# Performance work log

Measured on AMD Instinct MI355X. Metric: run time of the kernel, lower is better.

Reference implementation:

```python
import jax, jax.numpy as jnp
import numpy as np
import math

N = 100000      # nodes
DEG = 16        # fixed avg degree
E = N * DEG     # edges (nnz)
DIN = 128
DOUT = 32


def setup_inputs() -> dict:
    key = jax.random.key(0)
    k1, k2, k3, k4 = jax.random.split(key, 4)
    H = jax.random.normal(k1, (N, DIN), dtype=jnp.float32)
    stdv = 1.0 / math.sqrt(DOUT)
    weight = jax.random.uniform(k2, (DIN, DOUT), dtype=jnp.float32, minval=-stdv, maxval=stdv)
    # CSR adjacency: fixed degree per row -> rowPtr is an arithmetic sequence
    rowPtr = (jnp.arange(N + 1, dtype=jnp.int32) * DEG)
    colIdx = jax.random.randint(k3, (E,), 0, N, dtype=jnp.int32)
    val = jax.random.uniform(k4, (E,), dtype=jnp.float32)  # normalized edge weights
    return {"H": H, "weight": weight, "rowPtr": rowPtr, "colIdx": colIdx, "val": val}


def reference(H, weight, rowPtr, colIdx, val):
    # GCN layer: H' = A @ (H @ W), A sparse in CSR.
    HW = H @ weight                                   # [N, DOUT] dense GEMM
    n_rows = rowPtr.shape[0] - 1
    deg = jnp.diff(rowPtr)
    # expand CSR rowPtr to per-edge row ids (static total length -> jit-safe)
    rows = jnp.repeat(jnp.arange(n_rows, dtype=jnp.int32), deg,
                      total_repeat_length=colIdx.shape[0])
    msgs = HW[colIdx] * val[:, None]                  # [E, DOUT] gather + scale
    return jax.ops.segment_sum(msgs, rows, num_segments=n_rows)  # SpMM scatter-add
```

## Files before the change

kernel.cpp:

```cpp
#include <hip/hip_runtime.h>

#define DIN  128
#define DOUT 32

typedef __attribute__((ext_vector_type(8))) short bf16x8;
typedef __attribute__((ext_vector_type(4))) float f32x4;

__device__ __forceinline__ unsigned int f2b(float f) {
    unsigned int u = __float_as_uint(f);
    return (u + 0x7fffu + ((u >> 16) & 1u)) >> 16;
}
__device__ __forceinline__ unsigned int cvtpk(float lo, float hi) {
    unsigned int r;
    asm("v_cvt_pk_bf16_f32 %0, %1, %2" : "=v"(r) : "v"(lo), "v"(hi));
    return r;
}

union FragU { bf16x8 v; unsigned int u[4]; };

__global__ __launch_bounds__(256) void gemm_mfma_kernel(
    const float* __restrict__ H, const float* __restrict__ W,
    unsigned short* __restrict__ HWb, int n)
{
    const int lane = threadIdx.x & 63;
    const int w    = threadIdx.x >> 6;
    int rb = blockIdx.x * 128 + w * 32;
    if (rb + 32 > n) rb = n - 32;
    const int lr = lane & 15;
    const int kh = lane >> 4;

    bf16x8 bfrag[2][4];
    #pragma unroll
    for (int ct = 0; ct < 2; ++ct) {
        #pragma unroll
        for (int ks = 0; ks < 4; ++ks) {
            const int col = ct * 16 + lr;
            const int k0  = ks * 32 + kh * 8;
            float f[8];
            #pragma unroll
            for (int j = 0; j < 8; ++j) f[j] = W[(k0 + j) * DOUT + col];
            FragU fu;
            fu.u[0] = cvtpk(f[0], f[1]); fu.u[1] = cvtpk(f[2], f[3]);
            fu.u[2] = cvtpk(f[4], f[5]); fu.u[3] = cvtpk(f[6], f[7]);
            bfrag[ct][ks] = fu.v;
        }
    }

    f32x4 acc[2][2];
    #pragma unroll
    for (int rt = 0; rt < 2; ++rt)
        #pragma unroll
        for (int ct = 0; ct < 2; ++ct)
            acc[rt][ct] = (f32x4){0.f, 0.f, 0.f, 0.f};

    #pragma unroll
    for (int rt = 0; rt < 2; ++rt) {
        const float* __restrict__ hp = H + (size_t)(rb + rt * 16 + lr) * DIN;
        bf16x8 afrag[4];
        #pragma unroll
        for (int ks = 0; ks < 4; ++ks) {
            const int k0 = ks * 32 + kh * 8;
            const float4 lo = *reinterpret_cast<const float4*>(hp + k0);
            const float4 hi = *reinterpret_cast<const float4*>(hp + k0 + 4);
            FragU fu;
            fu.u[0] = cvtpk(lo.x, lo.y); fu.u[1] = cvtpk(lo.z, lo.w);
            fu.u[2] = cvtpk(hi.x, hi.y); fu.u[3] = cvtpk(hi.z, hi.w);
            afrag[ks] = fu.v;
        }
        #pragma unroll
        for (int ct = 0; ct < 2; ++ct)
            #pragma unroll
            for (int ks = 0; ks < 4; ++ks)
                acc[rt][ct] = __builtin_amdgcn_mfma_f32_16x16x32_bf16(
                    afrag[ks], bfrag[ct][ks], acc[rt][ct], 0, 0, 0);
    }

    #pragma unroll
    for (int rt = 0; rt < 2; ++rt) {
        #pragma unroll
        for (int ct = 0; ct < 2; ++ct) {
            #pragma unroll
            for (int r = 0; r < 4; ++r) {
                const int row = rb + rt * 16 + kh * 4 + r;
                const int col = ct * 16 + lr;
                HWb[(size_t)row * DOUT + col] = (unsigned short)f2b(acc[rt][ct][r]);
            }
        }
    }
}

__global__ __launch_bounds__(256) void spmm_kernel(
    const unsigned short* __restrict__ HWb, const int* __restrict__ rowPtr,
    const int* __restrict__ colIdx, const float* __restrict__ val,
    float* __restrict__ out, int n)
{
    const uint4* __restrict__ tbl = reinterpret_cast<const uint4*>(HWb);
    const int gid = blockIdx.x * 256 + threadIdx.x;
    const int row = gid >> 2;
    if (row >= n) return;
    const int cg = gid & 3;

    const int start = rowPtr[row];
    const int end   = rowPtr[row + 1];
    float a0=0,a1=0,a2=0,a3=0,a4=0,a5=0,a6=0,a7=0;

    #define BLO(u) __uint_as_float((u) << 16)
    #define BHI(u) __uint_as_float((u) & 0xffff0000u)
    #define STEP(E) {                                                        \
        const int   c_ = colIdx[E];                                          \
        const float v_ = val[E];                                             \
        const uint4 h_ = tbl[(size_t)c_ * 4 + cg];                           \
        a0 = fmaf(v_, BLO(h_.x), a0); a1 = fmaf(v_, BHI(h_.x), a1);          \
        a2 = fmaf(v_, BLO(h_.y), a2); a3 = fmaf(v_, BHI(h_.y), a3);          \
        a4 = fmaf(v_, BLO(h_.z), a4); a5 = fmaf(v_, BHI(h_.z), a5);          \
        a6 = fmaf(v_, BLO(h_.w), a6); a7 = fmaf(v_, BHI(h_.w), a7); }

    int e = start;
    for (; e + 8 <= end; e += 8) {
        STEP(e + 0) STEP(e + 1) STEP(e + 2) STEP(e + 3)
        STEP(e + 4) STEP(e + 5) STEP(e + 6) STEP(e + 7)
    }
    for (; e < end; ++e) { STEP(e) }
    #undef STEP
    #undef BLO
    #undef BHI

    float4* __restrict__ op =
        reinterpret_cast<float4*>(out) + (size_t)row * (DOUT / 4) + cg * 2;
    op[0] = make_float4(a0, a1, a2, a3);
    op[1] = make_float4(a4, a5, a6, a7);
}

__global__ __launch_bounds__(256) void fused_kernel(
    const float* __restrict__ H, const float* __restrict__ W,
    const int* __restrict__ rowPtr, const int* __restrict__ colIdx,
    const float* __restrict__ val, float* __restrict__ out, int n)
{
    __shared__ float Wlds[DIN * DOUT];
    for (int i = threadIdx.x; i < DIN * DOUT; i += 256) Wlds[i] = W[i];
    __syncthreads();

    const int gid = blockIdx.x * 256 + threadIdx.x;
    const int row = gid >> 5;
    if (row >= n) return;
    const int c = gid & 31;

    const int start = rowPtr[row];
    const int end   = rowPtr[row + 1];
    float acc = 0.f;
    for (int e = start; e < end; ++e) {
        const int   cidx = colIdx[e];
        const float v    = val[e];
        const float* h = H + (size_t)cidx * DIN;
        float dot = 0.f;
        #pragma unroll 8
        for (int k = 0; k < DIN; ++k)
            dot = fmaf(h[k], Wlds[k * DOUT + c], dot);
        acc = fmaf(v, dot, acc);
    }
    out[(size_t)row * DOUT + c] = acc;
}

extern "C" void kernel_launch(void* const* d_in, const int* in_sizes, int n_in,
                              void* d_out, int out_size, void* d_ws, size_t ws_size,
                              hipStream_t stream)
{
    const float* H      = (const float*)d_in[0];
    const float* W      = (const float*)d_in[1];
    const int*   rowPtr = (const int*)d_in[2];
    const int*   colIdx = (const int*)d_in[3];
    const float* val    = (const float*)d_in[4];
    float*       out    = (float*)d_out;

    const int n = in_sizes[2] - 1;
    const size_t hw_bytes = (size_t)n * DOUT * sizeof(unsigned short);

    if (ws_size >= hw_bytes && n >= 32) {
        unsigned short* HWb = (unsigned short*)d_ws;
        gemm_mfma_kernel<<<(n + 127) / 128, 256, 0, stream>>>(H, W, HWb, n);
        const int spmm_blocks = (int)(((size_t)n * 4 + 255) / 256);
        spmm_kernel<<<spmm_blocks, 256, 0, stream>>>(HWb, rowPtr, colIdx, val, out, n);
    } else {
        const int blocks = (int)(((size_t)n * DOUT + 255) / 256);
        fused_kernel<<<blocks, 256, 0, stream>>>(H, W, rowPtr, colIdx, val, out, n);
    }
}
```

Before: 39.42 us.

## Stage CSR indices in LDS and widen SpMM thread-per-row split; shrink GEMM tile

The GEMM kernel now gives each wave 16 rows instead of 32, which doubles the block count for more parallelism but reloads the W fragments twice as often. The SpMM kernel now processes 32 rows per block with 8 threads per row, each gathering 8-byte bf16 chunks. The block cooperatively stages colIdx and val for its edge range into shared memory, so the per-edge index loads come from LDS instead of repeated global loads. The cost is added synchronization and narrower gathers, in exchange for more threads per row and coalesced index loading.

```diff
diff --git a/kernel.cpp b/kernel.cpp
--- a/kernel.cpp
+++ b/kernel.cpp
@@ -24,8 +24,8 @@
 {
     const int lane = threadIdx.x & 63;
     const int w    = threadIdx.x >> 6;
-    int rb = blockIdx.x * 128 + w * 32;
-    if (rb + 32 > n) rb = n - 32;
+    int rb = blockIdx.x * 64 + w * 16;
+    if (rb + 16 > n) rb = n - 16;
     const int lr = lane & 15;
     const int kh = lane >> 4;
 
@@ -46,89 +46,97 @@
         }
     }
 
-    f32x4 acc[2][2];
+    const float* __restrict__ hp = H + (size_t)(rb + lr) * DIN;
+    bf16x8 afrag[4];
     #pragma unroll
-    for (int rt = 0; rt < 2; ++rt)
+    for (int ks = 0; ks < 4; ++ks) {
+        const int k0 = ks * 32 + kh * 8;
+        const float4 lo = *reinterpret_cast<const float4*>(hp + k0);
+        const float4 hi = *reinterpret_cast<const float4*>(hp + k0 + 4);
+        FragU fu;
+        fu.u[0] = cvtpk(lo.x, lo.y); fu.u[1] = cvtpk(lo.z, lo.w);
+        fu.u[2] = cvtpk(hi.x, hi.y); fu.u[3] = cvtpk(hi.z, hi.w);
+        afrag[ks] = fu.v;
+    }
+
+    f32x4 acc[2] = {(f32x4){0.f,0.f,0.f,0.f}, (f32x4){0.f,0.f,0.f,0.f}};
+    #pragma unroll
+    for (int ct = 0; ct < 2; ++ct)
         #pragma unroll
-        for (int ct = 0; ct < 2; ++ct)
-            acc[rt][ct] = (f32x4){0.f, 0.f, 0.f, 0.f};
+        for (int ks = 0; ks < 4; ++ks)
+            acc[ct] = __builtin_amdgcn_mfma_f32_16x16x32_bf16(
+                afrag[ks], bfrag[ct][ks], acc[ct], 0, 0, 0);
 
     #pragma unroll
-    for (int rt = 0; rt < 2; ++rt) {
-        const float* __restrict__ hp = H + (size_t)(rb + rt * 16 + lr) * DIN;
-        bf16x8 afrag[4];
+    for (int ct = 0; ct < 2; ++ct) {
         #pragma unroll
-        for (int ks = 0; ks < 4; ++ks) {
-            const int k0 = ks * 32 + kh * 8;
-            const float4 lo = *reinterpret_cast<const float4*>(hp + k0);
-            const float4 hi = *reinterpret_cast<const float4*>(hp + k0 + 4);
-            FragU fu;
-            fu.u[0] = cvtpk(lo.x, lo.y); fu.u[1] = cvtpk(lo.z, lo.w);
-            fu.u[2] = cvtpk(hi.x, hi.y); fu.u[3] = cvtpk(hi.z, hi.w);
-            afrag[ks] = fu.v;
-        }
-        #pragma unroll
-        for (int ct = 0; ct < 2; ++ct)
-            #pragma unroll
-            for (int ks = 0; ks < 4; ++ks)
-                acc[rt][ct] = __builtin_amdgcn_mfma_f32_16x16x32_bf16(
-                    afrag[ks], bfrag[ct][ks], acc[rt][ct], 0, 0, 0);
-    }
-
-    #pragma unroll
-    for (int rt = 0; rt < 2; ++rt) {
-        #pragma unroll
-        for (int ct = 0; ct < 2; ++ct) {
-            #pragma unroll
-            for (int r = 0; r < 4; ++r) {
-                const int row = rb + rt * 16 + kh * 4 + r;
-                const int col = ct * 16 + lr;
-                HWb[(size_t)row * DOUT + col] = (unsigned short)f2b(acc[rt][ct][r]);
-            }
+        for (int r = 0; r < 4; ++r) {
+            const int row = rb + kh * 4 + r;
+            const int col = ct * 16 + lr;
+            HWb[(size_t)row * DOUT + col] = (unsigned short)f2b(acc[ct][r]);
         }
     }
 }
 
+#define SROWS 32
 __global__ __launch_bounds__(256) void spmm_kernel(
     const unsigned short* __restrict__ HWb, const int* __restrict__ rowPtr,
     const int* __restrict__ colIdx, const float* __restrict__ val,
     float* __restrict__ out, int n)
 {
-    const uint4* __restrict__ tbl = reinterpret_cast<const uint4*>(HWb);
-    const int gid = blockIdx.x * 256 + threadIdx.x;
-    const int row = gid >> 2;
-    if (row >= n) return;
-    const int cg = gid & 3;
+    __shared__ int   sPtr[SROWS + 1];
+    __shared__ int   sIdx[1024];
+    __shared__ float sVal[1024];
 
-    const int start = rowPtr[row];
-    const int end   = rowPtr[row + 1];
-    float a0=0,a1=0,a2=0,a3=0,a4=0,a5=0,a6=0,a7=0;
+    const uint2* __restrict__ tbl = reinterpret_cast<const uint2*>(HWb);
+    const int tid = threadIdx.x;
+    const int r0  = blockIdx.x * SROWS;
 
-    #define BLO(u) __uint_as_float((u) << 16)
-    #define BHI(u) __uint_as_float((u) & 0xffff0000u)
-    #define STEP(E) {                                                        \
-        const int   c_ = colIdx[E];                                          \
-        const float v_ = val[E];                                             \
-        const uint4 h_ = tbl[(size_t)c_ * 4 + cg];                           \
-        a0 = fmaf(v_, BLO(h_.x), a0); a1 = fmaf(v_, BHI(h_.x), a1);          \
-        a2 = fmaf(v_, BLO(h_.y), a2); a3 = fmaf(v_, BHI(h_.y), a3);          \
-        a4 = fmaf(v_, BLO(h_.z), a4); a5 = fmaf(v_, BHI(h_.z), a5);          \
-        a6 = fmaf(v_, BLO(h_.w), a6); a7 = fmaf(v_, BHI(h_.w), a7); }
+    if (tid <= SROWS) {
+        int rr = r0 + tid;
+        if (rr > n) rr = n;
+        sPtr[tid] = rowPtr[rr];
+    }
+    __syncthreads();
 
-    int e = start;
-    for (; e + 8 <= end; e += 8) {
-        STEP(e + 0) STEP(e + 1) STEP(e + 2) STEP(e + 3)
-        STEP(e + 4) STEP(e + 5) STEP(e + 6) STEP(e + 7)
+    const int eBase0 = sPtr[0];
+    const int eEnd   = sPtr[SROWS];
+    const int lrow   = tid >> 3;
+    const int cg     = tid & 7;
+    const int row    = r0 + lrow;
+    const bool active = row < n;
+    const int myS = active ? sPtr[lrow]     : 0;
+    const int myE = active ? sPtr[lrow + 1] : 0;
+
+    float a0 = 0.f, a1 = 0.f, a2 = 0.f, a3 = 0.f;
+
+    for (int base = eBase0; base < eEnd; base += 1024) {
+        const int cnt = min(1024, eEnd - base);
+        if (base != eBase0) __syncthreads();
+        for (int i = tid; i < cnt; i += 256) {
+            sIdx[i] = colIdx[base + i];
+            sVal[i] = val[base + i];
+        }
+        __syncthreads();
+
+        const int js = max(myS, base) - base;
+        const int je = min(myE, base + cnt) - base;
+        #pragma unroll 8
+        for (int j = js; j < je; ++j) {
+            const int   c = sIdx[j];
+            const float v = sVal[j];
+            const uint2 g = tbl[(size_t)c * 8 + cg];
+            a0 = fmaf(v, __uint_as_float(g.x << 16), a0);
+            a1 = fmaf(v, __uint_as_float(g.x & 0xffff0000u), a1);
+            a2 = fmaf(v, __uint_as_float(g.y << 16), a2);
+            a3 = fmaf(v, __uint_as_float(g.y & 0xffff0000u), a3);
+        }
     }
-    for (; e < end; ++e) { STEP(e) }
-    #undef STEP
-    #undef BLO
-    #undef BHI
 
-    float4* __restrict__ op =
-        reinterpret_cast<float4*>(out) + (size_t)row * (DOUT / 4) + cg * 2;
-    op[0] = make_float4(a0, a1, a2, a3);
-    op[1] = make_float4(a4, a5, a6, a7);
+    if (active) {
+        reinterpret_cast<float4*>(out)[(size_t)row * (DOUT / 4) + cg] =
+            make_float4(a0, a1, a2, a3);
+    }
 }
 
 __global__ __launch_bounds__(256) void fused_kernel(
@@ -175,10 +183,10 @@
     const int n = in_sizes[2] - 1;
     const size_t hw_bytes = (size_t)n * DOUT * sizeof(unsigned short);
 
-    if (ws_size >= hw_bytes && n >= 32) {
+    if (ws_size >= hw_bytes && n >= 16) {
         unsigned short* HWb = (unsigned short*)d_ws;
-        gemm_mfma_kernel<<<(n + 127) / 128, 256, 0, stream>>>(H, W, HWb, n);
-        const int spmm_blocks = (int)(((size_t)n * 4 + 255) / 256);
+        gemm_mfma_kernel<<<(n + 63) / 64, 256, 0, stream>>>(H, W, HWb, n);
+        const int spmm_blocks = (n + SROWS - 1) / SROWS;
         spmm_kernel<<<spmm_blocks, 256, 0, stream>>>(HWb, rowPtr, colIdx, val, out, n);
     } else {
         const int blocks = (int)(((size_t)n * DOUT + 255) / 256);
```

New measurement: 38.01 us. 1.04x faster.
